# Kernel tuning notes

Measured on AMD Instinct MI355X. Metric: run time of the kernel, lower is better.

Reference implementation:

```python
import jax, jax.numpy as jnp
import numpy as np

DIM = 1024
NUM_HEADS = 16
HEAD_DIM = DIM // NUM_HEADS
SCALE = HEAD_DIM ** -0.5


def setup_inputs() -> dict:
    key = jax.random.key(0)
    k_x, k_qw, k_qb, k_pw, k_pb = jax.random.split(key, 5)
    B, N = 4, 4096
    x = jax.random.normal(k_x, (B, N, DIM), dtype=jnp.float32)
    # nn.Linear(dim, 3*dim): weight (out, in), bias (out,)
    s = DIM ** -0.5
    qkv_w = jax.random.uniform(k_qw, (3 * DIM, DIM), jnp.float32, -s, s)
    qkv_b = jax.random.uniform(k_qb, (3 * DIM,), jnp.float32, -s, s)
    proj_w = jax.random.uniform(k_pw, (DIM, DIM), jnp.float32, -s, s)
    proj_b = jax.random.uniform(k_pb, (DIM,), jnp.float32, -s, s)
    return {"x": x, "qkv_w": qkv_w, "qkv_b": qkv_b,
            "proj_w": proj_w, "proj_b": proj_b}


def reference(x, qkv_w, qkv_b, proj_w, proj_b):
    B, N, C = x.shape
    H, D = NUM_HEADS, HEAD_DIM
    # qkv projection: (B,N,3C) -> (B,N,3,H,D)
    qkv = (jnp.einsum('bnc,oc->bno', x, qkv_w) + qkv_b).reshape(B, N, 3, H, D)
    q, k, v = qkv[:, :, 0], qkv[:, :, 1], qkv[:, :, 2]  # each (B,N,H,D)
    # Faithful to source: matmul over the last two dims of (B,N,H,D),
    # i.e. attention scores over the HEAD axis per token -> (B,N,H,H).
    attn = jnp.einsum('bnhd,bngd->bnhg', q, k) * SCALE
    attn = jax.nn.softmax(attn, axis=-1)
    out = jnp.einsum('bnhg,bngd->bnhd', attn, v)      # (B,N,H,D)
    # torch: .transpose(1,2).reshape(B,N,C) -> (B,H,N,D) reshaped to (B,N,C)
    out = out.transpose(0, 2, 1, 3).reshape(B, N, C)
    return jnp.einsum('bnc,oc->bno', out, proj_w) + proj_b
```

## Files before the change

### kernel.cpp

```cpp
#include <hip/hip_runtime.h>
#include <hip/hip_bf16.h>

#define TOK   16384
#define KD    1024
#define NQKV  3072
#define SEQL  4096
#define ATT_SCALE 0.125f

typedef __attribute__((ext_vector_type(4))) float f32x4;
typedef __attribute__((ext_vector_type(8))) short bf16x8;

__device__ __forceinline__ unsigned short f2b(float f){
    union { float f; unsigned u; } x; x.f = f;
    return (unsigned short)((x.u + 0x7FFFu + ((x.u >> 16) & 1u)) >> 16);
}
__device__ __forceinline__ float b2f(unsigned short s){
    union { unsigned u; float f; } x; x.u = ((unsigned)s) << 16;
    return x.f;
}
__device__ __forceinline__ bf16x8 lds8(const unsigned short* p){
    union { uint4 u; bf16x8 v; } t; t.u = *(const uint4*)p; return t.v;
}
__device__ __forceinline__ void glds16(const void* g, void* l){
    __builtin_amdgcn_global_load_lds((const __attribute__((address_space(1))) unsigned*)g,
                                     (__attribute__((address_space(3))) unsigned*)l, 16, 0, 0);
}

__global__ __launch_bounds__(256) void cvt_kernel(const float* __restrict__ in,
                                                  unsigned short* __restrict__ out, int n)
{
    int i = (blockIdx.x * 256 + threadIdx.x) * 8;
    if (i >= n) return;
    float4 a = *(const float4*)(in + i);
    float4 b = *(const float4*)(in + i + 4);
    union { unsigned short u[8]; uint4 v; } t;
    t.u[0]=f2b(a.x); t.u[1]=f2b(a.y); t.u[2]=f2b(a.z); t.u[3]=f2b(a.w);
    t.u[4]=f2b(b.x); t.u[5]=f2b(b.y); t.u[6]=f2b(b.z); t.u[7]=f2b(b.w);
    *(uint4*)(out + i) = t.v;
}

template<bool OUT_BF16>
__global__ __launch_bounds__(512, 2) void gemm256(const unsigned short* __restrict__ A,
        const unsigned short* __restrict__ Bw, const float* __restrict__ bias,
        void* __restrict__ Cp, int Nn)
{
    extern __shared__ unsigned short smem[];
    unsigned short* As = smem;
    unsigned short* Bs = smem + 32768;

    const int tid = threadIdx.x, lane = tid & 63;
    const int w = tid >> 6, wm = w >> 2, wn = w & 3;
    const int rl = lane & 15, kslot = lane >> 4;

    const int gx = gridDim.x;
    const int nwg = gx * gridDim.y;
    int id = blockIdx.y * gx + blockIdx.x;
    id = (id & 7) * (nwg >> 3) + (id >> 3);
    const int cBase = (id % gx) * 256;
    const int mBase = (id / gx) * 256;

    const int u = tid >> 3;
    const int seg8 = ((tid & 7) ^ (u & 7)) * 8;
    const unsigned short* Ag = A  + (size_t)(mBase + u) * KD + seg8;
    const unsigned short* Bg = Bw + (size_t)(cBase + (u >> 4) * 64 + (u & 15)) * KD + seg8;

    const int arow = (wm * 16 + rl) * 64;
    const int brow = (wn * 16 + rl) * 64;
    const int psg0 = (kslot ^ (rl & 7)) * 8;
    const int psg1 = ((kslot + 4) ^ (rl & 7)) * 8;

    f32x4 acc[8][4];
    #pragma unroll
    for (int m = 0; m < 8; m++)
        #pragma unroll
        for (int n = 0; n < 4; n++) acc[m][n] = (f32x4)0.f;

#define STAGE_AH0(bb, kk) { glds16(Ag + (kk),            As + (bb)*16384 + tid*8); \
                            glds16(Ag + 64*KD + (kk),    As + (bb)*16384 + 4096  + tid*8); }
#define STAGE_AH1(bb, kk) { glds16(Ag + 128*KD + (kk),   As + (bb)*16384 + 8192  + tid*8); \
                            glds16(Ag + 192*KD + (kk),   As + (bb)*16384 + 12288 + tid*8); }
#define STAGE_BH0(bb, kk) { glds16(Bg + (kk),            Bs + (bb)*16384 + tid*8); \
                            glds16(Bg + 16*KD + (kk),    Bs + (bb)*16384 + 4096  + tid*8); }
#define STAGE_BH1(bb, kk) { glds16(Bg + 32*KD + (kk),    Bs + (bb)*16384 + 8192  + tid*8); \
                            glds16(Bg + 48*KD + (kk),    Bs + (bb)*16384 + 12288 + tid*8); }

#define RDA(a_, half) { _Pragma("unroll") \
    for (int m = 0; m < 4; m++) { \
        af[m][0] = lds8((a_) + (half)*8192 + arow + m*2048 + psg0); \
        af[m][1] = lds8((a_) + (half)*8192 + arow + m*2048 + psg1); } }
#define RDB(b_, nlo) { _Pragma("unroll") \
    for (int n = 0; n < 2; n++) { \
        bf[(nlo)+n][0] = lds8((b_) + brow + ((nlo)+n)*4096 + psg0); \
        bf[(nlo)+n][1] = lds8((b_) + brow + ((nlo)+n)*4096 + psg1); } }

#define MM16(mb, nb) { \
    __builtin_amdgcn_s_setprio(1); \
    _Pragma("unroll") \
    for (int m = 0; m < 4; m++) \
        _Pragma("unroll") \
        for (int n = 0; n < 2; n++) { \
            acc[(mb)+m][(nb)+n] = __builtin_amdgcn_mfma_f32_16x16x32_bf16(af[m][0], bf[(nb)+n][0], acc[(mb)+m][(nb)+n], 0, 0, 0); \
            acc[(mb)+m][(nb)+n] = __builtin_amdgcn_mfma_f32_16x16x32_bf16(af[m][1], bf[(nb)+n][1], acc[(mb)+m][(nb)+n], 0, 0, 0); } \
    __builtin_amdgcn_s_setprio(0); }

#define WAITLGKM { asm volatile("s_waitcnt lgkmcnt(0)" ::: "memory"); __builtin_amdgcn_sched_barrier(0); }

    bf16x8 af[4][2], bf[4][2];

    STAGE_AH0(0, 0)
    STAGE_BH0(0, 0)
    STAGE_BH1(0, 0)
    STAGE_AH1(0, 0)

    int buf = 0;
    for (int t = 0; t < 15; ++t) {
        const unsigned short* a = As + buf * 16384;
        const unsigned short* b = Bs + buf * 16384;
        const int nk = (t + 1) * 64;
        STAGE_AH0(buf ^ 1, nk)
        asm volatile("s_waitcnt vmcnt(6)" ::: "memory");
        __builtin_amdgcn_s_barrier();
        RDA(a, 0) RDB(b, 0)
        WAITLGKM
        MM16(0, 0)
        STAGE_BH0(buf ^ 1, nk)
        asm volatile("s_waitcnt vmcnt(6)" ::: "memory");
        __builtin_amdgcn_s_barrier();
        RDB(b, 2)
        WAITLGKM
        MM16(0, 2)
        STAGE_BH1(buf ^ 1, nk)
        asm volatile("s_waitcnt vmcnt(6)" ::: "memory");
        __builtin_amdgcn_s_barrier();
        RDA(a, 1)
        WAITLGKM
        MM16(4, 0)
        STAGE_AH1(buf ^ 1, nk)
        MM16(4, 2)
        buf ^= 1;
    }
    {
        const unsigned short* a = As + buf * 16384;
        const unsigned short* b = Bs + buf * 16384;
        asm volatile("s_waitcnt vmcnt(4)" ::: "memory");
        __builtin_amdgcn_s_barrier();
        RDA(a, 0) RDB(b, 0)
        WAITLGKM
        MM16(0, 0)
        asm volatile("s_waitcnt vmcnt(2)" ::: "memory");
        __builtin_amdgcn_s_barrier();
        RDB(b, 2)
        WAITLGKM
        MM16(0, 2)
        asm volatile("s_waitcnt vmcnt(0)" ::: "memory");
        __builtin_amdgcn_s_barrier();
        RDA(a, 1)
        WAITLGKM
        MM16(4, 0)
        MM16(4, 2)
    }
#undef STAGE_AH0
#undef STAGE_AH1
#undef STAGE_BH0
#undef STAGE_BH1
#undef RDA
#undef RDB
#undef MM16
#undef WAITLGKM

    float bv[4];
    #pragma unroll
    for (int n = 0; n < 4; n++) bv[n] = bias[cBase + wn * 64 + n * 16 + rl];
    #pragma unroll
    for (int m = 0; m < 8; m++) {
        #pragma unroll
        for (int i = 0; i < 4; i++) {
            const size_t row = mBase + (m >> 2) * 128 + (m & 3) * 32 + wm * 16 + kslot * 4 + i;
            #pragma unroll
            for (int n = 0; n < 4; n++) {
                const int col = cBase + wn * 64 + n * 16 + rl;
                const float val = acc[m][n][i] + bv[n];
                if (OUT_BF16) ((unsigned short*)Cp)[row * Nn + col] = f2b(val);
                else          ((float*)Cp)[row * Nn + col] = val;
            }
        }
    }
}

__global__ __launch_bounds__(256) void attn_kernel(const unsigned short* __restrict__ qkv,
                                                   unsigned short* __restrict__ outp)
{
    __shared__ __align__(16) unsigned short qs[4][48 * 72];
    __shared__ float ps[4][16 * 17];
    const int tid = threadIdx.x, w = tid >> 6, lane = tid & 63;
    const int t = blockIdx.x * 4 + w;

    const unsigned short* src = qkv + (size_t)t * NQKV;
    #pragma unroll
    for (int i = 0; i < 6; i++) {
        const int e = i * 512 + lane * 8;
        uint4 v = *(const uint4*)(src + e);
        *(uint4*)&qs[w][(e >> 6) * 72 + (e & 63)] = v;
    }
    __syncthreads();

    const int h = lane & 15, g0 = lane >> 4;
    uint4 qv[8];
    #pragma unroll
    for (int i = 0; i < 8; i++) qv[i] = *(const uint4*)&qs[w][h * 72 + i * 8];
    float s[4];
    #pragma unroll
    for (int i = 0; i < 4; i++) {
        const int g = g0 * 4 + i;
        float a = 0.f;
        #pragma unroll
        for (int c = 0; c < 8; c++) {
            uint4 kv = *(const uint4*)&qs[w][(16 + g) * 72 + c * 8];
            uint qa[4] = {qv[c].x, qv[c].y, qv[c].z, qv[c].w};
            uint ka[4] = {kv.x, kv.y, kv.z, kv.w};
            #pragma unroll
            for (int uu = 0; uu < 4; uu++) {
                a += b2f((unsigned short)qa[uu]) * b2f((unsigned short)ka[uu]);
                a += b2f((unsigned short)(qa[uu] >> 16)) * b2f((unsigned short)(ka[uu] >> 16));
            }
        }
        s[i] = a * ATT_SCALE;
    }
    float mx = fmaxf(fmaxf(s[0], s[1]), fmaxf(s[2], s[3]));
    mx = fmaxf(mx, __shfl_xor(mx, 16, 64));
    mx = fmaxf(mx, __shfl_xor(mx, 32, 64));
    float p[4], smv = 0.f;
    #pragma unroll
    for (int i = 0; i < 4; i++) { p[i] = __expf(s[i] - mx); smv += p[i]; }
    smv += __shfl_xor(smv, 16, 64);
    smv += __shfl_xor(smv, 32, 64);
    const float inv = 1.f / smv;
    #pragma unroll
    for (int i = 0; i < 4; i++) ps[w][h * 17 + g0 * 4 + i] = p[i] * inv;
    __syncthreads();

    const int h2 = lane >> 2, db = (lane & 3) * 16;
    float pr[16];
    #pragma unroll
    for (int g = 0; g < 16; g++) pr[g] = ps[w][h2 * 17 + g];
    float acc[16];
    #pragma unroll
    for (int j = 0; j < 16; j++) acc[j] = 0.f;
    #pragma unroll
    for (int g = 0; g < 16; g++) {
        const unsigned short* vp = &qs[w][(32 + g) * 72 + db];
        uint4 v0 = *(const uint4*)vp;
        uint4 v1 = *(const uint4*)(vp + 8);
        const float pg = pr[g];
        uint va[8] = {v0.x, v0.y, v0.z, v0.w, v1.x, v1.y, v1.z, v1.w};
        #pragma unroll
        for (int uu = 0; uu < 8; uu++) {
            acc[2*uu]   += pg * b2f((unsigned short)va[uu]);
            acc[2*uu+1] += pg * b2f((unsigned short)(va[uu] >> 16));
        }
    }
    const int b = t >> 12, n = t & 4095;
    const int n1 = h2 * 256 + (n >> 4);
    const int c0 = (n & 15) * 64 + db;
    union { unsigned short u[16]; uint4 v[2]; } st;
    #pragma unroll
    for (int j = 0; j < 16; j++) st.u[j] = f2b(acc[j]);
    unsigned short* dst = outp + ((size_t)(b * SEQL + n1)) * 1024 + c0;
    *(uint4*)dst       = st.v[0];
    *(uint4*)(dst + 8) = st.v[1];
}

extern "C" void kernel_launch(void* const* d_in, const int* in_sizes, int n_in,
                              void* d_out, int out_size, void* d_ws, size_t ws_size,
                              hipStream_t stream)
{
    const float* x      = (const float*)d_in[0];
    const float* qkv_w  = (const float*)d_in[1];
    const float* qkv_b  = (const float*)d_in[2];
    const float* proj_w = (const float*)d_in[3];
    const float* proj_b = (const float*)d_in[4];

    unsigned short* xb  = (unsigned short*)d_ws;
    unsigned short* qkv = xb + (size_t)TOK * KD;
    unsigned short* qwb = qkv + (size_t)TOK * NQKV;
    unsigned short* pwb = qwb + (size_t)NQKV * KD;
    unsigned short* att = xb;

    hipFuncSetAttribute(reinterpret_cast<const void*>(&gemm256<true>),
                        hipFuncAttributeMaxDynamicSharedMemorySize, 131072);
    hipFuncSetAttribute(reinterpret_cast<const void*>(&gemm256<false>),
                        hipFuncAttributeMaxDynamicSharedMemorySize, 131072);

    cvt_kernel<<<dim3(TOK * KD / 2048), dim3(256), 0, stream>>>(x, xb, TOK * KD);
    cvt_kernel<<<dim3(NQKV * KD / 2048), dim3(256), 0, stream>>>(qkv_w, qwb, NQKV * KD);
    cvt_kernel<<<dim3(KD * KD / 2048), dim3(256), 0, stream>>>(proj_w, pwb, KD * KD);

    gemm256<true><<<dim3(NQKV / 256, TOK / 256), dim3(512), 131072, stream>>>(
        xb, qwb, qkv_b, qkv, NQKV);
    attn_kernel<<<dim3(TOK / 4), dim3(256), 0, stream>>>(qkv, att);
    gemm256<false><<<dim3(KD / 256, TOK / 256), dim3(512), 131072, stream>>>(
        att, pwb, proj_b, (float*)d_out, KD);
}
```

Measured before the change: 201.1 us.

## Software-pipeline LDS fragment reads ahead of MFMA in GEMM main loop

Restructures the GEMM inner loop so LDS reads of B and A fragments for the next sub-step (and the next k-tile) are issued before the current MFMA block. Split B fragment registers into two sets (P/Q), so reads of one set overlap with MFMA on the other. Partial lgkmcnt waits replace full waits. The aim is to hide LDS latency behind matrix math. In exchange it adds more barriers and more live registers, and the reworked hazards between reads and stage writes could cause stalls or races.

```diff
diff --git a/kernel.cpp b/kernel.cpp
--- a/kernel.cpp
+++ b/kernel.cpp
@@ -88,85 +88,103 @@
     for (int m = 0; m < 4; m++) { \
         af[m][0] = lds8((a_) + (half)*8192 + arow + m*2048 + psg0); \
         af[m][1] = lds8((a_) + (half)*8192 + arow + m*2048 + psg1); } }
-#define RDB(b_, nlo) { _Pragma("unroll") \
+#define RDBP(b_) { _Pragma("unroll") \
     for (int n = 0; n < 2; n++) { \
-        bf[(nlo)+n][0] = lds8((b_) + brow + ((nlo)+n)*4096 + psg0); \
-        bf[(nlo)+n][1] = lds8((b_) + brow + ((nlo)+n)*4096 + psg1); } }
-
-#define MM16(mb, nb) { \
+        bfP[n][0] = lds8((b_) + brow + n*4096 + psg0); \
+        bfP[n][1] = lds8((b_) + brow + n*4096 + psg1); } }
+#define RDBQ(b_) { _Pragma("unroll") \
+    for (int n = 0; n < 2; n++) { \
+        bfQ[n][0] = lds8((b_) + brow + (2+n)*4096 + psg0); \
+        bfQ[n][1] = lds8((b_) + brow + (2+n)*4096 + psg1); } }
+
+#define MM(mb, nb, BF) { \
     __builtin_amdgcn_s_setprio(1); \
     _Pragma("unroll") \
     for (int m = 0; m < 4; m++) \
         _Pragma("unroll") \
         for (int n = 0; n < 2; n++) { \
-            acc[(mb)+m][(nb)+n] = __builtin_amdgcn_mfma_f32_16x16x32_bf16(af[m][0], bf[(nb)+n][0], acc[(mb)+m][(nb)+n], 0, 0, 0); \
-            acc[(mb)+m][(nb)+n] = __builtin_amdgcn_mfma_f32_16x16x32_bf16(af[m][1], bf[(nb)+n][1], acc[(mb)+m][(nb)+n], 0, 0, 0); } \
+            acc[(mb)+m][(nb)+n] = __builtin_amdgcn_mfma_f32_16x16x32_bf16(af[m][0], BF[n][0], acc[(mb)+m][(nb)+n], 0, 0, 0); \
+            acc[(mb)+m][(nb)+n] = __builtin_amdgcn_mfma_f32_16x16x32_bf16(af[m][1], BF[n][1], acc[(mb)+m][(nb)+n], 0, 0, 0); } \
     __builtin_amdgcn_s_setprio(0); }
 
-#define WAITLGKM { asm volatile("s_waitcnt lgkmcnt(0)" ::: "memory"); __builtin_amdgcn_sched_barrier(0); }
-
-    bf16x8 af[4][2], bf[4][2];
+#define VMC(N)  asm volatile("s_waitcnt vmcnt(" #N ")" ::: "memory");
+#define LGK(N)  asm volatile("s_waitcnt lgkmcnt(" #N ")" ::: "memory");
+#define BAR()   __builtin_amdgcn_s_barrier();
+
+    bf16x8 af[4][2], bfP[2][2], bfQ[2][2];
 
     STAGE_AH0(0, 0)
     STAGE_BH0(0, 0)
     STAGE_BH1(0, 0)
     STAGE_AH1(0, 0)
+    VMC(4)
+    BAR()
+    RDA(As, 0)
+    RDBP(Bs)
 
     int buf = 0;
     for (int t = 0; t < 15; ++t) {
         const unsigned short* a = As + buf * 16384;
         const unsigned short* b = Bs + buf * 16384;
+        const unsigned short* an = As + (buf ^ 1) * 16384;
+        const unsigned short* bn = Bs + (buf ^ 1) * 16384;
         const int nk = (t + 1) * 64;
         STAGE_AH0(buf ^ 1, nk)
-        asm volatile("s_waitcnt vmcnt(6)" ::: "memory");
-        __builtin_amdgcn_s_barrier();
-        RDA(a, 0) RDB(b, 0)
-        WAITLGKM
-        MM16(0, 0)
+        VMC(4)
+        BAR()
+        RDBQ(b)
+        LGK(4)
+        MM(0, 0, bfP)
+        BAR()
         STAGE_BH0(buf ^ 1, nk)
-        asm volatile("s_waitcnt vmcnt(6)" ::: "memory");
-        __builtin_amdgcn_s_barrier();
-        RDB(b, 2)
-        WAITLGKM
-        MM16(0, 2)
+        VMC(4)
+        BAR()
+        LGK(0)
+        MM(0, 2, bfQ)
+        RDA(a, 1)
+        BAR()
         STAGE_BH1(buf ^ 1, nk)
-        asm volatile("s_waitcnt vmcnt(6)" ::: "memory");
-        __builtin_amdgcn_s_barrier();
-        RDA(a, 1)
-        WAITLGKM
-        MM16(4, 0)
+        BAR()
+        LGK(0)
+        MM(4, 0, bfP)
+        BAR()
         STAGE_AH1(buf ^ 1, nk)
-        MM16(4, 2)
+        VMC(4)
+        BAR()
+        RDBP(bn)
+        MM(4, 2, bfQ)
+        RDA(an, 0)
+        BAR()
         buf ^= 1;
     }
     {
         const unsigned short* a = As + buf * 16384;
         const unsigned short* b = Bs + buf * 16384;
-        asm volatile("s_waitcnt vmcnt(4)" ::: "memory");
-        __builtin_amdgcn_s_barrier();
-        RDA(a, 0) RDB(b, 0)
-        WAITLGKM
-        MM16(0, 0)
-        asm volatile("s_waitcnt vmcnt(2)" ::: "memory");
-        __builtin_amdgcn_s_barrier();
-        RDB(b, 2)
-        WAITLGKM
-        MM16(0, 2)
-        asm volatile("s_waitcnt vmcnt(0)" ::: "memory");
-        __builtin_amdgcn_s_barrier();
+        VMC(2)
+        BAR()
+        RDBQ(b)
+        LGK(4)
+        MM(0, 0, bfP)
+        VMC(0)
+        BAR()
+        LGK(0)
+        MM(0, 2, bfQ)
         RDA(a, 1)
-        WAITLGKM
-        MM16(4, 0)
-        MM16(4, 2)
+        LGK(0)
+        MM(4, 0, bfP)
+        MM(4, 2, bfQ)
     }
 #undef STAGE_AH0
 #undef STAGE_AH1
 #undef STAGE_BH0
 #undef STAGE_BH1
 #undef RDA
-#undef RDB
-#undef MM16
-#undef WAITLGKM
+#undef RDBP
+#undef RDBQ
+#undef MM
+#undef VMC
+#undef LGK
+#undef BAR
 
     float bv[4];
     #pragma unroll
```

Result: slower. 225.6 us (+12.2%).

## Switch GEMM to 32x32x16 bf16 MFMA tiles with remapped LDS layout

Applied to the files above, without the earlier changes.

The 256x256 GEMM tile now uses 32x32x16 MFMA instructions instead of 16x16x32. The B staging order, the LDS fragment addressing and the epilogue row/column mapping change to match. Each wave loads fewer, larger fragments, which cuts LDS read traffic per MFMA and the instruction count. The explicit lgkmcnt waits and sched barriers are removed and the compiler now inserts the waits, which may change how LDS reads overlap with compute.

```diff
diff --git a/kernel.cpp b/kernel.cpp
--- a/kernel.cpp
+++ b/kernel.cpp
@@ -7,7 +7,7 @@
 #define SEQL  4096
 #define ATT_SCALE 0.125f
 
-typedef __attribute__((ext_vector_type(4))) float f32x4;
+typedef __attribute__((ext_vector_type(16))) float f32x16;
 typedef __attribute__((ext_vector_type(8))) short bf16x8;
 
 __device__ __forceinline__ unsigned short f2b(float f){
@@ -50,7 +50,7 @@
 
     const int tid = threadIdx.x, lane = tid & 63;
     const int w = tid >> 6, wm = w >> 2, wn = w & 3;
-    const int rl = lane & 15, kslot = lane >> 4;
+    const int l31 = lane & 31, lh = lane >> 5, lx = lane & 7;
 
     const int gx = gridDim.x;
     const int nwg = gx * gridDim.y;
@@ -61,51 +61,53 @@
 
     const int u = tid >> 3;
     const int seg8 = ((tid & 7) ^ (u & 7)) * 8;
-    const unsigned short* Ag = A  + (size_t)(mBase + u) * KD + seg8;
-    const unsigned short* Bg = Bw + (size_t)(cBase + (u >> 4) * 64 + (u & 15)) * KD + seg8;
-
-    const int arow = (wm * 16 + rl) * 64;
-    const int brow = (wn * 16 + rl) * 64;
-    const int psg0 = (kslot ^ (rl & 7)) * 8;
-    const int psg1 = ((kslot + 4) ^ (rl & 7)) * 8;
-
-    f32x4 acc[8][4];
-    #pragma unroll
-    for (int m = 0; m < 8; m++)
+    const unsigned short* Ag = A + (size_t)(mBase + u) * KD + seg8;
+    const int bcol = ((u & 127) >> 5) * 64 + (u >> 7) * 32 + (u & 31);
+    const unsigned short* Bg = Bw + (size_t)(cBase + bcol) * KD + seg8;
+
+    const int arowbase = (wm * 64 + l31) * 64;
+    const int bbase    = (wn * 32 + l31) * 64;
+    int sgk[4];
+    #pragma unroll
+    for (int ks = 0; ks < 4; ks++) sgk[ks] = ((2 * ks + lh) ^ lx) * 8;
+
+    f32x16 acc[4][2];
+    #pragma unroll
+    for (int mf = 0; mf < 4; mf++)
         #pragma unroll
-        for (int n = 0; n < 4; n++) acc[m][n] = (f32x4)0.f;
+        for (int nf = 0; nf < 2; nf++) acc[mf][nf] = (f32x16)0.f;
 
 #define STAGE_AH0(bb, kk) { glds16(Ag + (kk),            As + (bb)*16384 + tid*8); \
                             glds16(Ag + 64*KD + (kk),    As + (bb)*16384 + 4096  + tid*8); }
 #define STAGE_AH1(bb, kk) { glds16(Ag + 128*KD + (kk),   As + (bb)*16384 + 8192  + tid*8); \
                             glds16(Ag + 192*KD + (kk),   As + (bb)*16384 + 12288 + tid*8); }
 #define STAGE_BH0(bb, kk) { glds16(Bg + (kk),            Bs + (bb)*16384 + tid*8); \
-                            glds16(Bg + 16*KD + (kk),    Bs + (bb)*16384 + 4096  + tid*8); }
+                            glds16(Bg + 128*KD + (kk),   Bs + (bb)*16384 + 4096  + tid*8); }
 #define STAGE_BH1(bb, kk) { glds16(Bg + 32*KD + (kk),    Bs + (bb)*16384 + 8192  + tid*8); \
-                            glds16(Bg + 48*KD + (kk),    Bs + (bb)*16384 + 12288 + tid*8); }
-
-#define RDA(a_, half) { _Pragma("unroll") \
-    for (int m = 0; m < 4; m++) { \
-        af[m][0] = lds8((a_) + (half)*8192 + arow + m*2048 + psg0); \
-        af[m][1] = lds8((a_) + (half)*8192 + arow + m*2048 + psg1); } }
-#define RDB(b_, nlo) { _Pragma("unroll") \
-    for (int n = 0; n < 2; n++) { \
-        bf[(nlo)+n][0] = lds8((b_) + brow + ((nlo)+n)*4096 + psg0); \
-        bf[(nlo)+n][1] = lds8((b_) + brow + ((nlo)+n)*4096 + psg1); } }
-
-#define MM16(mb, nb) { \
+                            glds16(Bg + 160*KD + (kk),   Bs + (bb)*16384 + 12288 + tid*8); }
+
+#define RDA(a_, mh) { _Pragma("unroll") \
+    for (int fa = 0; fa < 2; fa++) \
+        _Pragma("unroll") \
+        for (int ks = 0; ks < 4; ks++) \
+            af[fa][ks] = lds8((a_) + (mh)*8192 + arowbase + fa*2048 + sgk[ks]); }
+#define RDB(b_, nh, BF) { _Pragma("unroll") \
+    for (int ks = 0; ks < 4; ks++) \
+        BF[ks] = lds8((b_) + (nh)*8192 + bbase + sgk[ks]); }
+
+#define MM(mh, nh, BF) { \
     __builtin_amdgcn_s_setprio(1); \
     _Pragma("unroll") \
-    for (int m = 0; m < 4; m++) \
+    for (int ks = 0; ks < 4; ks++) \
         _Pragma("unroll") \
-        for (int n = 0; n < 2; n++) { \
-            acc[(mb)+m][(nb)+n] = __builtin_amdgcn_mfma_f32_16x16x32_bf16(af[m][0], bf[(nb)+n][0], acc[(mb)+m][(nb)+n], 0, 0, 0); \
-            acc[(mb)+m][(nb)+n] = __builtin_amdgcn_mfma_f32_16x16x32_bf16(af[m][1], bf[(nb)+n][1], acc[(mb)+m][(nb)+n], 0, 0, 0); } \
+        for (int fa = 0; fa < 2; fa++) \
+            acc[(mh)*2+fa][nh] = __builtin_amdgcn_mfma_f32_32x32x16_bf16(af[fa][ks], BF[ks], acc[(mh)*2+fa][nh], 0, 0, 0); \
     __builtin_amdgcn_s_setprio(0); }
 
-#define WAITLGKM { asm volatile("s_waitcnt lgkmcnt(0)" ::: "memory"); __builtin_amdgcn_sched_barrier(0); }
-
-    bf16x8 af[4][2], bf[4][2];
+#define VMC(N)  asm volatile("s_waitcnt vmcnt(" #N ")" ::: "memory");
+#define BARR    __builtin_amdgcn_s_barrier();
+
+    bf16x8 af[2][4], bfP[4], bfQ[4];
 
     STAGE_AH0(0, 0)
     STAGE_BH0(0, 0)
@@ -118,46 +120,40 @@
         const unsigned short* b = Bs + buf * 16384;
         const int nk = (t + 1) * 64;
         STAGE_AH0(buf ^ 1, nk)
-        asm volatile("s_waitcnt vmcnt(6)" ::: "memory");
-        __builtin_amdgcn_s_barrier();
-        RDA(a, 0) RDB(b, 0)
-        WAITLGKM
-        MM16(0, 0)
+        VMC(6)
+        BARR
+        RDA(a, 0) RDB(b, 0, bfP)
+        MM(0, 0, bfP)
         STAGE_BH0(buf ^ 1, nk)
-        asm volatile("s_waitcnt vmcnt(6)" ::: "memory");
-        __builtin_amdgcn_s_barrier();
-        RDB(b, 2)
-        WAITLGKM
-        MM16(0, 2)
+        VMC(6)
+        BARR
+        RDB(b, 1, bfQ)
+        MM(0, 1, bfQ)
         STAGE_BH1(buf ^ 1, nk)
-        asm volatile("s_waitcnt vmcnt(6)" ::: "memory");
-        __builtin_amdgcn_s_barrier();
+        VMC(6)
+        BARR
         RDA(a, 1)
-        WAITLGKM
-        MM16(4, 0)
+        MM(1, 0, bfP)
         STAGE_AH1(buf ^ 1, nk)
-        MM16(4, 2)
+        MM(1, 1, bfQ)
         buf ^= 1;
     }
     {
         const unsigned short* a = As + buf * 16384;
         const unsigned short* b = Bs + buf * 16384;
-        asm volatile("s_waitcnt vmcnt(4)" ::: "memory");
-        __builtin_amdgcn_s_barrier();
-        RDA(a, 0) RDB(b, 0)
-        WAITLGKM
-        MM16(0, 0)
-        asm volatile("s_waitcnt vmcnt(2)" ::: "memory");
-        __builtin_amdgcn_s_barrier();
-        RDB(b, 2)
-        WAITLGKM
-        MM16(0, 2)
-        asm volatile("s_waitcnt vmcnt(0)" ::: "memory");
-        __builtin_amdgcn_s_barrier();
+        VMC(4)
+        BARR
+        RDA(a, 0) RDB(b, 0, bfP)
+        MM(0, 0, bfP)
+        VMC(2)
+        BARR
+        RDB(b, 1, bfQ)
+        MM(0, 1, bfQ)
+        VMC(0)
+        BARR
         RDA(a, 1)
-        WAITLGKM
-        MM16(4, 0)
-        MM16(4, 2)
+        MM(1, 0, bfP)
+        MM(1, 1, bfQ)
     }
 #undef STAGE_AH0
 #undef STAGE_AH1
@@ -165,21 +161,23 @@
 #undef STAGE_BH1
 #undef RDA
 #undef RDB
-#undef MM16
-#undef WAITLGKM
-
-    float bv[4];
-    #pragma unroll
-    for (int n = 0; n < 4; n++) bv[n] = bias[cBase + wn * 64 + n * 16 + rl];
-    #pragma unroll
-    for (int m = 0; m < 8; m++) {
+#undef MM
+#undef VMC
+#undef BARR
+
+    float bv[2];
+    #pragma unroll
+    for (int nf = 0; nf < 2; nf++) bv[nf] = bias[cBase + wn * 64 + nf * 32 + l31];
+    #pragma unroll
+    for (int mf = 0; mf < 4; mf++) {
+        const int row0 = mBase + (mf >> 1) * 128 + wm * 64 + (mf & 1) * 32 + lh * 4;
         #pragma unroll
-        for (int i = 0; i < 4; i++) {
-            const size_t row = mBase + (m >> 2) * 128 + (m & 3) * 32 + wm * 16 + kslot * 4 + i;
+        for (int reg = 0; reg < 16; reg++) {
+            const size_t row = row0 + (reg & 3) + 8 * (reg >> 2);
             #pragma unroll
-            for (int n = 0; n < 4; n++) {
-                const int col = cBase + wn * 64 + n * 16 + rl;
-                const float val = acc[m][n][i] + bv[n];
+            for (int nf = 0; nf < 2; nf++) {
+                const int col = cBase + wn * 64 + nf * 32 + l31;
+                const float val = acc[mf][nf][reg] + bv[nf];
                 if (OUT_BF16) ((unsigned short*)Cp)[row * Nn + col] = f2b(val);
                 else          ((float*)Cp)[row * Nn + col] = val;
             }
```

After: 213.2 us. +6.1%, slower.

## Add 128-tile GEMM for projection, fuse conversions, double-buffer B fragments

Applied to the files above, without the earlier changes.

The three fp32-to-bf16 conversion launches are merged into one kernel that picks its source by block index, which saves two launches. A new 128x128-tile, 256-thread GEMM is used for the output projection (N=1024), so the grid has 1024 workgroups instead of 256 and fills the CUs better. Both GEMMs now keep B fragments in two register sets and drop the explicit lgkmcnt(0) waits, letting the compiler overlap LDS reads with MFMAs. The smaller tile has less data reuse per workgroup and uses more registers for the split fragments.

```diff
diff --git a/kernel.cpp b/kernel.cpp
--- a/kernel.cpp
+++ b/kernel.cpp
@@ -26,17 +26,23 @@
                                      (__attribute__((address_space(3))) unsigned*)l, 16, 0, 0);
 }
 
-__global__ __launch_bounds__(256) void cvt_kernel(const float* __restrict__ in,
-                                                  unsigned short* __restrict__ out, int n)
+__global__ __launch_bounds__(256) void cvt3_kernel(const float* __restrict__ x,
+        const float* __restrict__ qw, const float* __restrict__ pw,
+        unsigned short* __restrict__ xb, unsigned short* __restrict__ qwb,
+        unsigned short* __restrict__ pwb)
 {
-    int i = (blockIdx.x * 256 + threadIdx.x) * 8;
-    if (i >= n) return;
-    float4 a = *(const float4*)(in + i);
-    float4 b = *(const float4*)(in + i + 4);
+    const int b = blockIdx.x;
+    const float* src; unsigned short* dst; int off;
+    if (b < 8192)       { src = x;  dst = xb;  off = b; }
+    else if (b < 9728)  { src = qw; dst = qwb; off = b - 8192; }
+    else                { src = pw; dst = pwb; off = b - 9728; }
+    const int i = (off * 256 + threadIdx.x) * 8;
+    float4 a = *(const float4*)(src + i);
+    float4 c = *(const float4*)(src + i + 4);
     union { unsigned short u[8]; uint4 v; } t;
     t.u[0]=f2b(a.x); t.u[1]=f2b(a.y); t.u[2]=f2b(a.z); t.u[3]=f2b(a.w);
-    t.u[4]=f2b(b.x); t.u[5]=f2b(b.y); t.u[6]=f2b(b.z); t.u[7]=f2b(b.w);
-    *(uint4*)(out + i) = t.v;
+    t.u[4]=f2b(c.x); t.u[5]=f2b(c.y); t.u[6]=f2b(c.z); t.u[7]=f2b(c.w);
+    *(uint4*)(dst + i) = t.v;
 }
 
 template<bool OUT_BF16>
@@ -88,24 +94,25 @@
     for (int m = 0; m < 4; m++) { \
         af[m][0] = lds8((a_) + (half)*8192 + arow + m*2048 + psg0); \
         af[m][1] = lds8((a_) + (half)*8192 + arow + m*2048 + psg1); } }
-#define RDB(b_, nlo) { _Pragma("unroll") \
+#define RDB(b_, nlo, BF) { _Pragma("unroll") \
     for (int n = 0; n < 2; n++) { \
-        bf[(nlo)+n][0] = lds8((b_) + brow + ((nlo)+n)*4096 + psg0); \
-        bf[(nlo)+n][1] = lds8((b_) + brow + ((nlo)+n)*4096 + psg1); } }
-
-#define MM16(mb, nb) { \
+        BF[n][0] = lds8((b_) + brow + ((nlo)+n)*4096 + psg0); \
+        BF[n][1] = lds8((b_) + brow + ((nlo)+n)*4096 + psg1); } }
+
+#define MM16(mb, nb, BF) { \
     __builtin_amdgcn_s_setprio(1); \
     _Pragma("unroll") \
     for (int m = 0; m < 4; m++) \
         _Pragma("unroll") \
         for (int n = 0; n < 2; n++) { \
-            acc[(mb)+m][(nb)+n] = __builtin_amdgcn_mfma_f32_16x16x32_bf16(af[m][0], bf[(nb)+n][0], acc[(mb)+m][(nb)+n], 0, 0, 0); \
-            acc[(mb)+m][(nb)+n] = __builtin_amdgcn_mfma_f32_16x16x32_bf16(af[m][1], bf[(nb)+n][1], acc[(mb)+m][(nb)+n], 0, 0, 0); } \
+            acc[(mb)+m][(nb)+n] = __builtin_amdgcn_mfma_f32_16x16x32_bf16(af[m][0], BF[n][0], acc[(mb)+m][(nb)+n], 0, 0, 0); \
+            acc[(mb)+m][(nb)+n] = __builtin_amdgcn_mfma_f32_16x16x32_bf16(af[m][1], BF[n][1], acc[(mb)+m][(nb)+n], 0, 0, 0); } \
     __builtin_amdgcn_s_setprio(0); }
 
-#define WAITLGKM { asm volatile("s_waitcnt lgkmcnt(0)" ::: "memory"); __builtin_amdgcn_sched_barrier(0); }
-
-    bf16x8 af[4][2], bf[4][2];
+#define VMC(N)  asm volatile("s_waitcnt vmcnt(" #N ")" ::: "memory");
+#define BARR    __builtin_amdgcn_s_barrier();
+
+    bf16x8 af[4][2], bfP[2][2], bfQ[2][2];
 
     STAGE_AH0(0, 0)
     STAGE_BH0(0, 0)
@@ -118,46 +125,40 @@
         const unsigned short* b = Bs + buf * 16384;
         const int nk = (t + 1) * 64;
         STAGE_AH0(buf ^ 1, nk)
-        asm volatile("s_waitcnt vmcnt(6)" ::: "memory");
-        __builtin_amdgcn_s_barrier();
-        RDA(a, 0) RDB(b, 0)
-        WAITLGKM
-        MM16(0, 0)
+        VMC(6)
+        BARR
+        RDA(a, 0) RDB(b, 0, bfP)
+        MM16(0, 0, bfP)
         STAGE_BH0(buf ^ 1, nk)
-        asm volatile("s_waitcnt vmcnt(6)" ::: "memory");
-        __builtin_amdgcn_s_barrier();
-        RDB(b, 2)
-        WAITLGKM
-        MM16(0, 2)
+        VMC(6)
+        BARR
+        RDB(b, 2, bfQ)
+        MM16(0, 2, bfQ)
         STAGE_BH1(buf ^ 1, nk)
-        asm volatile("s_waitcnt vmcnt(6)" ::: "memory");
-        __builtin_amdgcn_s_barrier();
+        VMC(6)
+        BARR
         RDA(a, 1)
-        WAITLGKM
-        MM16(4, 0)
+        MM16(4, 0, bfP)
         STAGE_AH1(buf ^ 1, nk)
-        MM16(4, 2)
+        MM16(4, 2, bfQ)
         buf ^= 1;
     }
     {
         const unsigned short* a = As + buf * 16384;
         const unsigned short* b = Bs + buf * 16384;
-        asm volatile("s_waitcnt vmcnt(4)" ::: "memory");
-        __builtin_amdgcn_s_barrier();
-        RDA(a, 0) RDB(b, 0)
-        WAITLGKM
-        MM16(0, 0)
-        asm volatile("s_waitcnt vmcnt(2)" ::: "memory");
-        __builtin_amdgcn_s_barrier();
-        RDB(b, 2)
-        WAITLGKM
-        MM16(0, 2)
-        asm volatile("s_waitcnt vmcnt(0)" ::: "memory");
-        __builtin_amdgcn_s_barrier();
+        VMC(4)
+        BARR
+        RDA(a, 0) RDB(b, 0, bfP)
+        MM16(0, 0, bfP)
+        VMC(2)
+        BARR
+        RDB(b, 2, bfQ)
+        MM16(0, 2, bfQ)
+        VMC(0)
+        BARR
         RDA(a, 1)
-        WAITLGKM
-        MM16(4, 0)
-        MM16(4, 2)
+        MM16(4, 0, bfP)
+        MM16(4, 2, bfQ)
     }
 #undef STAGE_AH0
 #undef STAGE_AH1
@@ -166,7 +167,8 @@
 #undef RDA
 #undef RDB
 #undef MM16
-#undef WAITLGKM
+#undef VMC
+#undef BARR
 
     float bv[4];
     #pragma unroll
@@ -176,6 +178,151 @@
         #pragma unroll
         for (int i = 0; i < 4; i++) {
             const size_t row = mBase + (m >> 2) * 128 + (m & 3) * 32 + wm * 16 + kslot * 4 + i;
+            #pragma unroll
+            for (int n = 0; n < 4; n++) {
+                const int col = cBase + wn * 64 + n * 16 + rl;
+                const float val = acc[m][n][i] + bv[n];
+                if (OUT_BF16) ((unsigned short*)Cp)[row * Nn + col] = f2b(val);
+                else          ((float*)Cp)[row * Nn + col] = val;
+            }
+        }
+    }
+}
+
+template<bool OUT_BF16>
+__global__ __launch_bounds__(256, 2) void gemm128(const unsigned short* __restrict__ A,
+        const unsigned short* __restrict__ Bw, const float* __restrict__ bias,
+        void* __restrict__ Cp, int Nn)
+{
+    extern __shared__ unsigned short smem[];
+    unsigned short* As = smem;
+    unsigned short* Bs = smem + 16384;
+
+    const int tid = threadIdx.x, lane = tid & 63;
+    const int w = tid >> 6, wm = w >> 1, wn = w & 1;
+    const int rl = lane & 15, kslot = lane >> 4;
+
+    const int gx = gridDim.x;
+    const int nwg = gx * gridDim.y;
+    int id = blockIdx.y * gx + blockIdx.x;
+    id = (id & 7) * (nwg >> 3) + (id >> 3);
+    const int cBase = (id % gx) * 128;
+    const int mBase = (id / gx) * 128;
+
+    const int u = tid >> 3;
+    const int seg8 = ((tid & 7) ^ (u & 7)) * 8;
+    const unsigned short* Ag = A + (size_t)(mBase + u) * KD + seg8;
+    const int bq = ((u >> 4) & 1) * 16 + (u & 15);
+    const unsigned short* Bg = Bw + (size_t)(cBase + bq) * KD + seg8;
+
+    const int arow = wm * 2048 + rl * 64;
+    const int brow = wn * 2048 + rl * 64;
+    const int psg0 = (kslot ^ (rl & 7)) * 8;
+    const int psg1 = ((kslot + 4) ^ (rl & 7)) * 8;
+
+    f32x4 acc[4][4];
+    #pragma unroll
+    for (int m = 0; m < 4; m++)
+        #pragma unroll
+        for (int n = 0; n < 4; n++) acc[m][n] = (f32x4)0.f;
+
+#define STAGE_AH0(bb, kk) { glds16(Ag + (kk),           As + (bb)*8192 + tid*8); \
+                            glds16(Ag + 32*KD + (kk),   As + (bb)*8192 + 2048 + tid*8); }
+#define STAGE_AH1(bb, kk) { glds16(Ag + 64*KD + (kk),   As + (bb)*8192 + 4096 + tid*8); \
+                            glds16(Ag + 96*KD + (kk),   As + (bb)*8192 + 6144 + tid*8); }
+#define STAGE_BH0(bb, kk) { glds16(Bg + (kk),           Bs + (bb)*8192 + tid*8); \
+                            glds16(Bg + 64*KD + (kk),   Bs + (bb)*8192 + 2048 + tid*8); }
+#define STAGE_BH1(bb, kk) { glds16(Bg + 32*KD + (kk),   Bs + (bb)*8192 + 4096 + tid*8); \
+                            glds16(Bg + 96*KD + (kk),   Bs + (bb)*8192 + 6144 + tid*8); }
+
+#define RDA(a_, half) { _Pragma("unroll") \
+    for (int q = 0; q < 2; q++) { \
+        af[q][0] = lds8((a_) + (half)*4096 + arow + q*1024 + psg0); \
+        af[q][1] = lds8((a_) + (half)*4096 + arow + q*1024 + psg1); } }
+#define RDB(b_, half, BF) { _Pragma("unroll") \
+    for (int q = 0; q < 2; q++) { \
+        BF[q][0] = lds8((b_) + (half)*4096 + brow + q*1024 + psg0); \
+        BF[q][1] = lds8((b_) + (half)*4096 + brow + q*1024 + psg1); } }
+
+#define MM8(mh, nh, BF) { \
+    __builtin_amdgcn_s_setprio(1); \
+    _Pragma("unroll") \
+    for (int qa = 0; qa < 2; qa++) \
+        _Pragma("unroll") \
+        for (int qb = 0; qb < 2; qb++) { \
+            acc[(mh)*2+qa][(nh)*2+qb] = __builtin_amdgcn_mfma_f32_16x16x32_bf16(af[qa][0], BF[qb][0], acc[(mh)*2+qa][(nh)*2+qb], 0, 0, 0); \
+            acc[(mh)*2+qa][(nh)*2+qb] = __builtin_amdgcn_mfma_f32_16x16x32_bf16(af[qa][1], BF[qb][1], acc[(mh)*2+qa][(nh)*2+qb], 0, 0, 0); } \
+    __builtin_amdgcn_s_setprio(0); }
+
+#define VMC(N)  asm volatile("s_waitcnt vmcnt(" #N ")" ::: "memory");
+#define BARR    __builtin_amdgcn_s_barrier();
+
+    bf16x8 af[2][2], bfP[2][2], bfQ[2][2];
+
+    STAGE_AH0(0, 0)
+    STAGE_BH0(0, 0)
+    STAGE_BH1(0, 0)
+    STAGE_AH1(0, 0)
+
+    int buf = 0;
+    for (int t = 0; t < 15; ++t) {
+        const unsigned short* a = As + buf * 8192;
+        const unsigned short* b = Bs + buf * 8192;
+        const int nk = (t + 1) * 64;
+        STAGE_AH0(buf ^ 1, nk)
+        VMC(6)
+        BARR
+        RDA(a, 0) RDB(b, 0, bfP)
+        MM8(0, 0, bfP)
+        STAGE_BH0(buf ^ 1, nk)
+        VMC(6)
+        BARR
+        RDB(b, 1, bfQ)
+        MM8(0, 1, bfQ)
+        STAGE_BH1(buf ^ 1, nk)
+        VMC(6)
+        BARR
+        RDA(a, 1)
+        MM8(1, 0, bfP)
+        STAGE_AH1(buf ^ 1, nk)
+        MM8(1, 1, bfQ)
+        buf ^= 1;
+    }
+    {
+        const unsigned short* a = As + buf * 8192;
+        const unsigned short* b = Bs + buf * 8192;
+        VMC(4)
+        BARR
+        RDA(a, 0) RDB(b, 0, bfP)
+        MM8(0, 0, bfP)
+        VMC(2)
+        BARR
+        RDB(b, 1, bfQ)
+        MM8(0, 1, bfQ)
+        VMC(0)
+        BARR
+        RDA(a, 1)
+        MM8(1, 0, bfP)
+        MM8(1, 1, bfQ)
+    }
+#undef STAGE_AH0
+#undef STAGE_AH1
+#undef STAGE_BH0
+#undef STAGE_BH1
+#undef RDA
+#undef RDB
+#undef MM8
+#undef VMC
+#undef BARR
+
+    float bv[4];
+    #pragma unroll
+    for (int n = 0; n < 4; n++) bv[n] = bias[cBase + wn * 64 + n * 16 + rl];
+    #pragma unroll
+    for (int m = 0; m < 4; m++) {
+        #pragma unroll
+        for (int i = 0; i < 4; i++) {
+            const size_t row = mBase + (m >> 1) * 64 + wm * 32 + (m & 1) * 16 + kslot * 4 + i;
             #pragma unroll
             for (int n = 0; n < 4; n++) {
                 const int col = cBase + wn * 64 + n * 16 + rl;
@@ -288,16 +435,14 @@
 
     hipFuncSetAttribute(reinterpret_cast<const void*>(&gemm256<true>),
                         hipFuncAttributeMaxDynamicSharedMemorySize, 131072);
-    hipFuncSetAttribute(reinterpret_cast<const void*>(&gemm256<false>),
-                        hipFuncAttributeMaxDynamicSharedMemorySize, 131072);
-
-    cvt_kernel<<<dim3(TOK * KD / 2048), dim3(256), 0, stream>>>(x, xb, TOK * KD);
-    cvt_kernel<<<dim3(NQKV * KD / 2048), dim3(256), 0, stream>>>(qkv_w, qwb, NQKV * KD);
-    cvt_kernel<<<dim3(KD * KD / 2048), dim3(256), 0, stream>>>(proj_w, pwb, KD * KD);
+    hipFuncSetAttribute(reinterpret_cast<const void*>(&gemm128<false>),
+                        hipFuncAttributeMaxDynamicSharedMemorySize, 65536);
+
+    cvt3_kernel<<<dim3(10240), dim3(256), 0, stream>>>(x, qkv_w, proj_w, xb, qwb, pwb);
 
     gemm256<true><<<dim3(NQKV / 256, TOK / 256), dim3(512), 131072, stream>>>(
         xb, qwb, qkv_b, qkv, NQKV);
     attn_kernel<<<dim3(TOK / 4), dim3(256), 0, stream>>>(qkv, att);
-    gemm256<false><<<dim3(KD / 256, TOK / 256), dim3(512), 131072, stream>>>(
+    gemm128<false><<<dim3(KD / 128, TOK / 128), dim3(256), 65536, stream>>>(
         att, pwb, proj_b, (float*)d_out, KD);
 }
```

Result: slower. 208.1 us (+3.5%).
